# Performance work log

Measured on AMD Instinct MI355X. Metric: run time of the kernel, lower is better.

The kernel has to match this reference:

```python
import jax, jax.numpy as jnp
import numpy as np

N, L, E, H = 4, 2048, 1024, 16
DK = E // H  # 64

def setup_inputs() -> dict:
    key = jax.random.key(0)
    ks = jax.random.split(key, 5)
    scale = 0.02
    return {
        "x": jax.random.normal(ks[0], (N, L, E), dtype=jnp.float32),
        "Wq": jax.random.normal(ks[1], (E, E), dtype=jnp.float32) * scale,
        "Wk": jax.random.normal(ks[2], (E, E), dtype=jnp.float32) * scale,
        "Wv": jax.random.normal(ks[3], (E, E), dtype=jnp.float32) * scale,
        "Wo": jax.random.normal(ks[4], (E, E), dtype=jnp.float32) * scale,
    }

def reference(x, Wq, Wk, Wv, Wo):
    n, l, _ = x.shape
    # nn.Linear(bias=False): y = x @ W.T
    q = x @ Wq.T  # (n, l, H*DK)
    k = x @ Wk.T
    v = x @ Wv.T
    # Faithful to torch .view: plain reshape (NOT transpose-based head split)
    q = q.reshape(n, H, l, DK)
    k = k.reshape(n, H, l, DK)
    v = v.reshape(n, H, l, DK)
    scores = jnp.einsum('nhqd,nhkd->nhqk', q, k) / jnp.sqrt(jnp.float32(DK))
    attn = jax.nn.softmax(scores, axis=-1)
    out = jnp.einsum('nhqk,nhkd->nhqd', attn, v).reshape(n, l, H * DK)
    return out @ Wo.T
```

## Files before the change

kernel.cpp:

```cpp
#include <hip/hip_runtime.h>


#define DEVI __device__ __forceinline__

typedef _Float16 half8 __attribute__((ext_vector_type(8)));
typedef _Float16 half4 __attribute__((ext_vector_type(4)));
typedef float f32x4 __attribute__((ext_vector_type(4)));

DEVI void gload_lds16(const void* g, void* l) {
    __builtin_amdgcn_global_load_lds(
        (const __attribute__((address_space(1))) void*)g,
        (__attribute__((address_space(3))) void*)l,
        16, 0, 0);
}

DEVI f32x4 zero4() { f32x4 z = {0.f, 0.f, 0.f, 0.f}; return z; }

#if __has_builtin(__builtin_amdgcn_exp2f)
DEVI float fast_exp2(float x) { return __builtin_amdgcn_exp2f(x); }
#else
DEVI float fast_exp2(float x) { return exp2f(x); }
#endif

#if __has_builtin(__builtin_amdgcn_mfma_f32_16x16x16f16)
DEVI f32x4 mfma16(half4 a, half4 b, f32x4 c) {
    return __builtin_amdgcn_mfma_f32_16x16x16f16(a, b, c, 0, 0, 0);
}
#else
DEVI f32x4 mfma16(half4 a, half4 b, f32x4 c) {
    asm volatile("v_mfma_f32_16x16x16_f16 %0, %1, %2, %0"
                 : "+v"(c) : "v"(a), "v"(b));
    return c;
}
#endif

DEVI half8 lds_read8_swz(const _Float16* base, int row, int colbyte) {
    const char* p = (const char*)base;
    const int off = (row * 128 + colbyte) ^ ((row & 7) << 4);
    return *(const half8*)(p + off);
}

__global__ __launch_bounds__(256) void f2h_kernel(const float* __restrict__ s,
                                                  _Float16* __restrict__ d) {
    const size_t i = (size_t)blockIdx.x * 256 + threadIdx.x;
    const float4 v = ((const float4*)s)[i];
    half4 h;
    h[0] = (_Float16)v.x; h[1] = (_Float16)v.y;
    h[2] = (_Float16)v.z; h[3] = (_Float16)v.w;
    ((half4*)d)[i] = h;
}

template<int MODE>
__global__ __launch_bounds__(256) void gemm_k(const _Float16* __restrict__ A,
                                              const _Float16* __restrict__ B,
                                              void* __restrict__ Cout,
                                              float qscale) {
    constexpr int NBLK = (MODE == 0) ? 24 : 8;
    constexpr int CPX  = (MODE == 0) ? 192 : 64;
    alignas(16) __shared__ _Float16 As[128 * 64];
    alignas(16) __shared__ _Float16 Bs[128 * 64];
    const int t = threadIdx.x;
    const int lane = t & 63;
    const int w = t >> 6;
    const int wr = (w >> 1) * 64;
    const int wc = (w & 1) * 64;
    const int nid = (blockIdx.x & 7) * CPX + (blockIdx.x >> 3);
    const int bn = (nid % NBLK) * 128;
    const int bm = (nid / NBLK) * 128;
    const int r16 = lane & 15;
    const int q4 = lane >> 4;
    const int sr = t >> 3;
    const int sc8 = ((t & 7) ^ (sr & 7)) * 8;

    f32x4 acc[4][4];
    #pragma unroll
    for (int mi = 0; mi < 4; ++mi)
        #pragma unroll
        for (int ni = 0; ni < 4; ++ni)
            acc[mi][ni] = zero4();

    for (int kt = 0; kt < 1024; kt += 64) {
        #pragma unroll
        for (int i = 0; i < 4; ++i) {
            gload_lds16(A + (size_t)(bm + i * 32 + sr) * 1024 + kt + sc8, &As[i * 2048 + t * 8]);
            gload_lds16(B + (size_t)(bn + i * 32 + sr) * 1024 + kt + sc8, &Bs[i * 2048 + t * 8]);
        }
        __syncthreads();
        #pragma unroll
        for (int kk = 0; kk < 2; ++kk) {
            half8 a[4], b[4];
            #pragma unroll
            for (int mi = 0; mi < 4; ++mi)
                a[mi] = lds_read8_swz(As, wr + mi * 16 + r16, (kk * 32 + q4 * 8) * 2);
            #pragma unroll
            for (int ni = 0; ni < 4; ++ni)
                b[ni] = lds_read8_swz(Bs, wc + ni * 16 + r16, (kk * 32 + q4 * 8) * 2);
            #pragma unroll
            for (int mi = 0; mi < 4; ++mi)
                #pragma unroll
                for (int ni = 0; ni < 4; ++ni)
                    acc[mi][ni] = __builtin_amdgcn_mfma_f32_16x16x32_f16(b[ni], a[mi], acc[mi][ni], 0, 0, 0);
        }
        __syncthreads();
    }
    if (MODE == 0) {
        const int which = bn >> 10;
        const int cb2 = bn & 1023;
        const float alpha = (which == 0) ? qscale : 1.0f;
        _Float16* C = (_Float16*)Cout + (size_t)which * 8388608;
        #pragma unroll
        for (int mi = 0; mi < 4; ++mi) {
            const int row = bm + wr + mi * 16 + r16;
            #pragma unroll
            for (int ni = 0; ni < 4; ++ni) {
                const int col0 = cb2 + wc + ni * 16 + q4 * 4;
                half4 ov;
                #pragma unroll
                for (int i = 0; i < 4; ++i)
                    ov[i] = (_Float16)(acc[mi][ni][i] * alpha);
                *(half4*)&C[(size_t)row * 1024 + col0] = ov;
            }
        }
    } else {
        float* C = (float*)Cout;
        #pragma unroll
        for (int mi = 0; mi < 4; ++mi) {
            const int row = bm + wr + mi * 16 + r16;
            #pragma unroll
            for (int ni = 0; ni < 4; ++ni) {
                const int col0 = bn + wc + ni * 16 + q4 * 4;
                *(f32x4*)&C[(size_t)row * 1024 + col0] = acc[mi][ni];
            }
        }
    }
}

__global__ __launch_bounds__(256) void repack_v(const _Float16* __restrict__ V,
                                                _Float16* __restrict__ V4) {
    __shared__ unsigned short lds[64 * 65];
    const int t = threadIdx.x;
    const int kt = blockIdx.x;
    const size_t hb = (size_t)blockIdx.y * 131072;
    const int r = t >> 2;
    const int c0 = (t & 3) * 16;
    const unsigned short* Vi = (const unsigned short*)V;
    #pragma unroll
    for (int jj = 0; jj < 2; ++jj) {
        union { uint4 u; unsigned short s[8]; } tmp;
        tmp.u = *(const uint4*)&Vi[hb + (size_t)(kt * 64 + r) * 64 + c0 + jj * 8];
        #pragma unroll
        for (int e = 0; e < 8; ++e)
            lds[r * 65 + c0 + jj * 8 + e] = tmp.s[e];
    }
    __syncthreads();
    const size_t ob = hb + (size_t)kt * 4096;
    const unsigned short* ls = lds;
    #pragma unroll
    for (int h = 0; h < 2; ++h) {
        half8 v;
        #pragma unroll
        for (int e = 0; e < 8; ++e) {
            const int idx = t * 16 + h * 8 + e;
            const int a = idx >> 8;
            const int d = (idx >> 2) & 63;
            const int j = idx & 3;
            unsigned short u = ls[(4 * a + j) * 65 + d];
            v[e] = *(const _Float16*)&u;
        }
        *(half8*)&V4[ob + t * 16 + h * 8] = v;
    }
}

__global__ __launch_bounds__(256) void attn_kernel(const _Float16* __restrict__ Q,
                                                   const _Float16* __restrict__ K,
                                                   const _Float16* __restrict__ V4,
                                                   _Float16* __restrict__ O) {
    alignas(16) __shared__ _Float16 Ks[2][64 * 64];
    alignas(16) __shared__ _Float16 Vs[2][64 * 64];
    const int t = threadIdx.x;
    const int lane = t & 63;
    const int w = t >> 6;
    const int nid = (blockIdx.x & 7) * 128 + (blockIdx.x >> 3);
    const size_t hb = (size_t)(nid >> 4) * 131072;
    const int qt = nid & 15;
    const int r16 = lane & 15;
    const int q4 = lane >> 4;
    const int sr = t >> 3;
    const int sc = t & 7;

    half8 aq[2][2];
    const int q0 = qt * 128 + w * 32;
    #pragma unroll
    for (int mi = 0; mi < 2; ++mi)
        #pragma unroll
        for (int kk = 0; kk < 2; ++kk)
            aq[mi][kk] = *(const half8*)&Q[hb + (size_t)(q0 + mi * 16 + r16) * 64 + kk * 32 + q4 * 8];

    f32x4 o[4][2];
    float lsum[2] = {0.f, 0.f};
    #pragma unroll
    for (int ni = 0; ni < 4; ++ni)
        #pragma unroll
        for (int mi = 0; mi < 2; ++mi)
            o[ni][mi] = zero4();

    const int R0 = sr, R1 = 32 + sr;
    const int scs0 = (sc ^ (R0 & 7)) * 8;
    const int scs1 = (sc ^ (R1 & 7)) * 8;

    {
        gload_lds16(&K[hb + (size_t)R0 * 64 + scs0],  &Ks[0][t * 8]);
        gload_lds16(&K[hb + (size_t)R1 * 64 + scs1],  &Ks[0][2048 + t * 8]);
        gload_lds16(&V4[hb + t * 8],                  &Vs[0][t * 8]);
        gload_lds16(&V4[hb + 2048 + t * 8],           &Vs[0][2048 + t * 8]);
    }
    __syncthreads();

    int pb = 0;
    for (int kt = 0; kt < 32; ++kt) {
        if (kt + 1 < 32) {
            const size_t tb = hb + (size_t)(kt + 1) * 4096;
            gload_lds16(&K[tb + (size_t)R0 * 64 + scs0],  &Ks[pb ^ 1][t * 8]);
            gload_lds16(&K[tb + (size_t)R1 * 64 + scs1],  &Ks[pb ^ 1][2048 + t * 8]);
            gload_lds16(&V4[tb + t * 8],                  &Vs[pb ^ 1][t * 8]);
            gload_lds16(&V4[tb + 2048 + t * 8],           &Vs[pb ^ 1][2048 + t * 8]);
        }

        f32x4 sT[4][2];
        #pragma unroll
        for (int ki = 0; ki < 4; ++ki)
            #pragma unroll
            for (int mi = 0; mi < 2; ++mi)
                sT[ki][mi] = zero4();
        __builtin_amdgcn_s_setprio(1);
        #pragma unroll
        for (int kk = 0; kk < 2; ++kk) {
            half8 ak[4];
            #pragma unroll
            for (int ki = 0; ki < 4; ++ki)
                ak[ki] = lds_read8_swz(Ks[pb], ki * 16 + r16, (kk * 32 + q4 * 8) * 2);
            #pragma unroll
            for (int ki = 0; ki < 4; ++ki)
                #pragma unroll
                for (int mi = 0; mi < 2; ++mi)
                    sT[ki][mi] = __builtin_amdgcn_mfma_f32_16x16x32_f16(ak[ki], aq[mi][kk], sT[ki][mi], 0, 0, 0);
        }
        __builtin_amdgcn_s_setprio(0);

        half4 pT[4][2];
        #pragma unroll
        for (int ki = 0; ki < 4; ++ki)
            #pragma unroll
            for (int mi = 0; mi < 2; ++mi) {
                const float p0 = fast_exp2(sT[ki][mi][0]);
                const float p1 = fast_exp2(sT[ki][mi][1]);
                const float p2 = fast_exp2(sT[ki][mi][2]);
                const float p3 = fast_exp2(sT[ki][mi][3]);
                lsum[mi] += (p0 + p1) + (p2 + p3);
                half4 pv;
                pv[0] = (_Float16)p0; pv[1] = (_Float16)p1;
                pv[2] = (_Float16)p2; pv[3] = (_Float16)p3;
                pT[ki][mi] = pv;
            }

        __builtin_amdgcn_s_setprio(1);
        #pragma unroll
        for (int ki = 0; ki < 4; ++ki)
            #pragma unroll
            for (int ni = 0; ni < 4; ++ni) {
                const half4 av = *(const half4*)&Vs[pb][(ki * 4 + q4) * 256 + (ni * 16 + r16) * 4];
                #pragma unroll
                for (int mi = 0; mi < 2; ++mi)
                    o[ni][mi] = mfma16(av, pT[ki][mi], o[ni][mi]);
            }
        __builtin_amdgcn_s_setprio(0);

        __syncthreads();
        pb ^= 1;
    }

    float inv[2];
    #pragma unroll
    for (int mi = 0; mi < 2; ++mi) {
        float l = lsum[mi];
        l += __shfl_xor(l, 16);
        l += __shfl_xor(l, 32);
        inv[mi] = 1.f / l;
    }
    #pragma unroll
    for (int mi = 0; mi < 2; ++mi) {
        const int q = q0 + mi * 16 + r16;
        #pragma unroll
        for (int ni = 0; ni < 4; ++ni) {
            half4 ov;
            #pragma unroll
            for (int i = 0; i < 4; ++i)
                ov[i] = (_Float16)(o[ni][mi][i] * inv[mi]);
            *(half4*)&O[hb + (size_t)q * 64 + ni * 16 + q4 * 4] = ov;
        }
    }
}

extern "C" void kernel_launch(void* const* d_in, const int* in_sizes, int n_in,
                              void* d_out, int out_size, void* d_ws, size_t ws_size,
                              hipStream_t stream) {
    const float* x  = (const float*)d_in[0];
    const float* Wq = (const float*)d_in[1];
    const float* Wk = (const float*)d_in[2];
    const float* Wv = (const float*)d_in[3];
    const float* Wo = (const float*)d_in[4];

    const size_t XSZ = (size_t)8192 * 1024;
    const size_t WSZ = (size_t)1024 * 1024;

    _Float16* ws  = (_Float16*)d_ws;
    _Float16* xh  = ws;
    _Float16* wqh = ws + XSZ;
    _Float16* wkh = wqh + WSZ;
    _Float16* wvh = wkh + WSZ;
    _Float16* woh = wvh + WSZ;
    _Float16* qh  = woh + WSZ;
    _Float16* kh  = qh + XSZ;
    _Float16* vh  = kh + XSZ;
    _Float16* aoh = vh + XSZ;
    _Float16* v4h = xh;

    f2h_kernel<<<XSZ / 4 / 256, 256, 0, stream>>>(x,  xh);
    f2h_kernel<<<WSZ / 4 / 256, 256, 0, stream>>>(Wq, wqh);
    f2h_kernel<<<WSZ / 4 / 256, 256, 0, stream>>>(Wk, wkh);
    f2h_kernel<<<WSZ / 4 / 256, 256, 0, stream>>>(Wv, wvh);
    f2h_kernel<<<WSZ / 4 / 256, 256, 0, stream>>>(Wo, woh);

    const float qscale = 0.125f * 1.44269504088896340736f;

    gemm_k<0><<<1536, 256, 0, stream>>>(xh, wqh, (void*)qh, qscale);

    repack_v<<<dim3(32, 64), 256, 0, stream>>>(vh, v4h);

    attn_kernel<<<1024, 256, 0, stream>>>(qh, kh, v4h, aoh);

    gemm_k<1><<<512, 256, 0, stream>>>(aoh, woh, d_out, 1.0f);
    (void)in_sizes; (void)n_in; (void)out_size; (void)ws_size;
}
```

Measured before the change: 318.9 us.

## Replace QKV projection GEMM with 256x256 double-buffered 8-wave pipelined kernel

The fused QKV projection GEMM now uses 512-thread blocks computing 256x256 tiles. LDS is double-buffered and split into half-tiles so the next k-tile's global-to-LDS loads are issued in stages between MFMA phases, with explicit waitcnt, barriers and setprio. This aims to hide load latency and raise data reuse per block. The output GEMM is split into its own kernel that drops the LDS swizzle, swaps MFMA operand order and writes scalar column-wise stores, which may cause LDS bank conflicts and less coalesced stores.

```diff
diff --git a/kernel.cpp b/kernel.cpp
--- a/kernel.cpp
+++ b/kernel.cpp
@@ -50,13 +50,151 @@
     ((half4*)d)[i] = h;
 }
 
-template<int MODE>
-__global__ __launch_bounds__(256) void gemm_k(const _Float16* __restrict__ A,
-                                              const _Float16* __restrict__ B,
-                                              void* __restrict__ Cout,
-                                              float qscale) {
-    constexpr int NBLK = (MODE == 0) ? 24 : 8;
-    constexpr int CPX  = (MODE == 0) ? 192 : 64;
+__global__ __launch_bounds__(512, 2) void gemm8(const _Float16* __restrict__ A,
+                                                const _Float16* __restrict__ B,
+                                                _Float16* __restrict__ Cout,
+                                                float qscale) {
+    alignas(16) __shared__ _Float16 Al[2][2][128 * 64];
+    alignas(16) __shared__ _Float16 Bl[2][2][128 * 64];
+    const int t = threadIdx.x;
+    const int lane = t & 63;
+    const int w = t >> 6;
+    const int wm = w >> 2;
+    const int wn = w & 3;
+    const int bh = wn >> 1;
+    const int brow0 = (wn & 1) * 64;
+    const int r16 = lane & 15;
+    const int q4 = lane >> 4;
+    const int nid = (blockIdx.x & 7) * 48 + (blockIdx.x >> 3);
+    const int bn = (nid % 12) * 256;
+    const int bm = (nid / 12) * 256;
+    const int srow = t >> 3;
+    const int scol = ((t & 7) ^ (srow & 7)) * 8;
+
+    f32x4 acc[8][4];
+    #pragma unroll
+    for (int mi = 0; mi < 8; ++mi)
+        #pragma unroll
+        for (int ni = 0; ni < 4; ++ni)
+            acc[mi][ni] = zero4();
+
+    auto stageH = [&](int kind, int ktile) {
+        const int d = ktile & 1;
+        const int h = kind >> 1;
+        const bool isB = kind & 1;
+        const _Float16* src = isB ? B : A;
+        const int baseRow = (isB ? bn : bm) + h * 128;
+        _Float16* dst = isB ? &Bl[d][h][0] : &Al[d][h][0];
+        #pragma unroll
+        for (int i = 0; i < 2; ++i)
+            gload_lds16(src + (size_t)(baseRow + i * 64 + srow) * 1024 + ktile * 64 + scol,
+                        dst + i * 4096 + t * 8);
+    };
+
+    stageH(0, 0); stageH(1, 0); stageH(2, 0); stageH(3, 0);
+
+    for (int kt = 0; kt < 16; ++kt) {
+        const int d = kt & 1;
+        const _Float16* Ah = &Al[d][wm][0];
+        const _Float16* Bh = &Bl[d][bh][0];
+        const bool pf = (kt < 15);
+        half8 af[4], bf[4];
+
+        if (pf) stageH(0, kt + 1);
+        if (pf) asm volatile("s_waitcnt vmcnt(2)" ::: "memory");
+        else    asm volatile("s_waitcnt vmcnt(0)" ::: "memory");
+        __builtin_amdgcn_sched_barrier(0);
+        __builtin_amdgcn_s_barrier();
+        __builtin_amdgcn_sched_barrier(0);
+        #pragma unroll
+        for (int mi = 0; mi < 4; ++mi)
+            af[mi] = lds_read8_swz(Ah, mi * 16 + r16, q4 * 16);
+        #pragma unroll
+        for (int ni = 0; ni < 4; ++ni)
+            bf[ni] = lds_read8_swz(Bh, brow0 + ni * 16 + r16, q4 * 16);
+        asm volatile("s_waitcnt lgkmcnt(0)" ::: "memory");
+        __builtin_amdgcn_sched_barrier(0);
+        __builtin_amdgcn_s_setprio(1);
+        #pragma unroll
+        for (int mi = 0; mi < 4; ++mi)
+            #pragma unroll
+            for (int ni = 0; ni < 4; ++ni)
+                acc[mi][ni] = __builtin_amdgcn_mfma_f32_16x16x32_f16(af[mi], bf[ni], acc[mi][ni], 0, 0, 0);
+        __builtin_amdgcn_s_setprio(0);
+        __builtin_amdgcn_s_barrier();
+
+        #pragma unroll
+        for (int mi = 0; mi < 4; ++mi)
+            af[mi] = lds_read8_swz(Ah, (4 + mi) * 16 + r16, q4 * 16);
+        if (pf) stageH(1, kt + 1);
+        __builtin_amdgcn_s_barrier();
+        asm volatile("s_waitcnt lgkmcnt(0)" ::: "memory");
+        __builtin_amdgcn_sched_barrier(0);
+        __builtin_amdgcn_s_setprio(1);
+        #pragma unroll
+        for (int mi = 0; mi < 4; ++mi)
+            #pragma unroll
+            for (int ni = 0; ni < 4; ++ni)
+                acc[4 + mi][ni] = __builtin_amdgcn_mfma_f32_16x16x32_f16(af[mi], bf[ni], acc[4 + mi][ni], 0, 0, 0);
+        __builtin_amdgcn_s_setprio(0);
+        __builtin_amdgcn_s_barrier();
+
+        #pragma unroll
+        for (int mi = 0; mi < 4; ++mi)
+            af[mi] = lds_read8_swz(Ah, mi * 16 + r16, 64 + q4 * 16);
+        #pragma unroll
+        for (int ni = 0; ni < 4; ++ni)
+            bf[ni] = lds_read8_swz(Bh, brow0 + ni * 16 + r16, 64 + q4 * 16);
+        if (pf) stageH(2, kt + 1);
+        __builtin_amdgcn_s_barrier();
+        asm volatile("s_waitcnt lgkmcnt(0)" ::: "memory");
+        __builtin_amdgcn_sched_barrier(0);
+        __builtin_amdgcn_s_setprio(1);
+        #pragma unroll
+        for (int mi = 0; mi < 4; ++mi)
+            #pragma unroll
+            for (int ni = 0; ni < 4; ++ni)
+                acc[mi][ni] = __builtin_amdgcn_mfma_f32_16x16x32_f16(af[mi], bf[ni], acc[mi][ni], 0, 0, 0);
+        __builtin_amdgcn_s_setprio(0);
+        __builtin_amdgcn_s_barrier();
+
+        #pragma unroll
+        for (int mi = 0; mi < 4; ++mi)
+            af[mi] = lds_read8_swz(Ah, (4 + mi) * 16 + r16, 64 + q4 * 16);
+        if (pf) stageH(3, kt + 1);
+        __builtin_amdgcn_s_barrier();
+        asm volatile("s_waitcnt lgkmcnt(0)" ::: "memory");
+        __builtin_amdgcn_sched_barrier(0);
+        __builtin_amdgcn_s_setprio(1);
+        #pragma unroll
+        for (int mi = 0; mi < 4; ++mi)
+            #pragma unroll
+            for (int ni = 0; ni < 4; ++ni)
+                acc[4 + mi][ni] = __builtin_amdgcn_mfma_f32_16x16x32_f16(af[mi], bf[ni], acc[4 + mi][ni], 0, 0, 0);
+        __builtin_amdgcn_s_setprio(0);
+        __builtin_amdgcn_s_barrier();
+    }
+
+    const int which = bn >> 10;
+    const int cb2 = bn & 1023;
+    const float alpha = (which == 0) ? qscale : 1.0f;
+    _Float16* C = Cout + (size_t)which * 8388608;
+    #pragma unroll
+    for (int mi = 0; mi < 8; ++mi) {
+        const int row = bm + wm * 128 + mi * 16 + q4 * 4;
+        #pragma unroll
+        for (int ni = 0; ni < 4; ++ni) {
+            const int col = cb2 + wn * 64 + ni * 16 + r16;
+            #pragma unroll
+            for (int i = 0; i < 4; ++i)
+                C[(size_t)(row + i) * 1024 + col] = (_Float16)(acc[mi][ni][i] * alpha);
+        }
+    }
+}
+
+__global__ __launch_bounds__(256) void gemm_wo(const _Float16* __restrict__ A,
+                                               const _Float16* __restrict__ B,
+                                               float* __restrict__ C) {
     alignas(16) __shared__ _Float16 As[128 * 64];
     alignas(16) __shared__ _Float16 Bs[128 * 64];
     const int t = threadIdx.x;
@@ -64,13 +202,13 @@
     const int w = t >> 6;
     const int wr = (w >> 1) * 64;
     const int wc = (w & 1) * 64;
-    const int nid = (blockIdx.x & 7) * CPX + (blockIdx.x >> 3);
-    const int bn = (nid % NBLK) * 128;
-    const int bm = (nid / NBLK) * 128;
+    const int nid = (blockIdx.x & 7) * 64 + (blockIdx.x >> 3);
+    const int bn = (nid % 8) * 128;
+    const int bm = (nid / 8) * 128;
     const int r16 = lane & 15;
     const int q4 = lane >> 4;
     const int sr = t >> 3;
-    const int sc8 = ((t & 7) ^ (sr & 7)) * 8;
+    const int sc8 = (t & 7) * 8;
 
     f32x4 acc[4][4];
     #pragma unroll
@@ -91,46 +229,27 @@
             half8 a[4], b[4];
             #pragma unroll
             for (int mi = 0; mi < 4; ++mi)
-                a[mi] = lds_read8_swz(As, wr + mi * 16 + r16, (kk * 32 + q4 * 8) * 2);
+                a[mi] = *(const half8*)&As[(wr + mi * 16 + r16) * 64 + kk * 32 + q4 * 8];
             #pragma unroll
             for (int ni = 0; ni < 4; ++ni)
-                b[ni] = lds_read8_swz(Bs, wc + ni * 16 + r16, (kk * 32 + q4 * 8) * 2);
+                b[ni] = *(const half8*)&Bs[(wc + ni * 16 + r16) * 64 + kk * 32 + q4 * 8];
             #pragma unroll
             for (int mi = 0; mi < 4; ++mi)
                 #pragma unroll
                 for (int ni = 0; ni < 4; ++ni)
-                    acc[mi][ni] = __builtin_amdgcn_mfma_f32_16x16x32_f16(b[ni], a[mi], acc[mi][ni], 0, 0, 0);
+                    acc[mi][ni] = __builtin_amdgcn_mfma_f32_16x16x32_f16(a[mi], b[ni], acc[mi][ni], 0, 0, 0);
         }
         __syncthreads();
     }
-    if (MODE == 0) {
-        const int which = bn >> 10;
-        const int cb2 = bn & 1023;
-        const float alpha = (which == 0) ? qscale : 1.0f;
-        _Float16* C = (_Float16*)Cout + (size_t)which * 8388608;
-        #pragma unroll
-        for (int mi = 0; mi < 4; ++mi) {
-            const int row = bm + wr + mi * 16 + r16;
-            #pragma unroll
-            for (int ni = 0; ni < 4; ++ni) {
-                const int col0 = cb2 + wc + ni * 16 + q4 * 4;
-                half4 ov;
-                #pragma unroll
-                for (int i = 0; i < 4; ++i)
-                    ov[i] = (_Float16)(acc[mi][ni][i] * alpha);
-                *(half4*)&C[(size_t)row * 1024 + col0] = ov;
-            }
-        }
-    } else {
-        float* C = (float*)Cout;
-        #pragma unroll
-        for (int mi = 0; mi < 4; ++mi) {
-            const int row = bm + wr + mi * 16 + r16;
-            #pragma unroll
-            for (int ni = 0; ni < 4; ++ni) {
-                const int col0 = bn + wc + ni * 16 + q4 * 4;
-                *(f32x4*)&C[(size_t)row * 1024 + col0] = acc[mi][ni];
-            }
+    #pragma unroll
+    for (int mi = 0; mi < 4; ++mi) {
+        const int row = bm + wr + mi * 16 + q4 * 4;
+        #pragma unroll
+        for (int ni = 0; ni < 4; ++ni) {
+            const int col = bn + wc + ni * 16 + r16;
+            #pragma unroll
+            for (int i = 0; i < 4; ++i)
+                C[(size_t)(row + i) * 1024 + col] = acc[mi][ni][i];
         }
     }
 }
@@ -333,12 +452,12 @@
 
     const float qscale = 0.125f * 1.44269504088896340736f;
 
-    gemm_k<0><<<1536, 256, 0, stream>>>(xh, wqh, (void*)qh, qscale);
+    gemm8<<<384, 512, 0, stream>>>(xh, wqh, qh, qscale);
 
     repack_v<<<dim3(32, 64), 256, 0, stream>>>(vh, v4h);
 
     attn_kernel<<<1024, 256, 0, stream>>>(qh, kh, v4h, aoh);
 
-    gemm_k<1><<<512, 256, 0, stream>>>(aoh, woh, d_out, 1.0f);
+    gemm_wo<<<512, 256, 0, stream>>>(aoh, woh, (float*)d_out);
     (void)in_sizes; (void)n_in; (void)out_size; (void)ws_size;
 }
```

Result: no change. 312.8 us (-1.9%).
